# Optimization experiments

Measured on AMD Instinct MI355X. Metric: run time of the kernel, lower is better.

The kernel has to match this reference:

```python
import jax, jax.numpy as jnp
import numpy as np

NUM_HEADS = 16
KEY_DIM = 64
NUM_FEATURES = 256
D_MODEL = NUM_HEADS * KEY_DIM
EPS = 1e-6


def softmax_kernel(data, proj):
    # data: [..., N, D], proj: [D, F]
    # Faithful to source: ratio uses proj.shape[0] (=D), matching the TF code.
    data_normalizer = 1.0 / jnp.sqrt(jnp.sqrt(jnp.asarray(data.shape[-1], data.dtype)))
    ratio = 1.0 / jnp.sqrt(jnp.asarray(proj.shape[0], data.dtype))
    data = data_normalizer * data
    data_dash = jnp.einsum('...nd,df->...nf', data, proj)
    diag = jnp.sum(jnp.square(data), axis=-1, keepdims=True)  # [..., N, 1]
    return ratio * (jnp.exp(data_dash - diag / 2.0) + EPS)


def setup_inputs() -> dict:
    key = jax.random.key(0)
    ks = jax.random.split(key, 12)
    B, N = 4, 4096
    s = 1.0 / np.sqrt(D_MODEL)
    inp = {
        'queries': jax.random.normal(ks[0], (B, N, D_MODEL), jnp.float32),
        'keys': jax.random.normal(ks[1], (B, N, D_MODEL), jnp.float32),
        'Wq': jax.random.normal(ks[2], (D_MODEL, D_MODEL), jnp.float32) * s,
        'bq': jnp.zeros((D_MODEL,), jnp.float32),
        'Wk': jax.random.normal(ks[3], (D_MODEL, D_MODEL), jnp.float32) * s,
        'bk': jnp.zeros((D_MODEL,), jnp.float32),
        'Wv': jax.random.normal(ks[4], (D_MODEL, D_MODEL), jnp.float32) * s,
        'bv': jnp.zeros((D_MODEL,), jnp.float32),
        'Wo': jax.random.normal(ks[5], (D_MODEL, D_MODEL), jnp.float32) * s,
        'bo': jnp.zeros((D_MODEL,), jnp.float32),
        # GlorotNormal for [KEY_DIM, NUM_FEATURES]
        'proj': jax.random.normal(ks[6], (KEY_DIM, NUM_FEATURES), jnp.float32)
                * np.sqrt(2.0 / (KEY_DIM + NUM_FEATURES)),
    }
    return inp


def reference(queries, keys, Wq, bq, Wk, bk, Wv, bv, Wo, bo, proj):
    # Original code uses x = queries for q, k, v (self-attention); keys arg unused.
    x = queries
    B, N, _ = x.shape
    H, D = NUM_HEADS, KEY_DIM

    def split_heads(t):
        return t.reshape(B, N, H, D).transpose(0, 2, 1, 3)  # [B,H,N,D]

    q = split_heads(x @ Wq + bq)
    k = split_heads(x @ Wk + bk)
    v = split_heads(x @ Wv + bv)

    q_prime = softmax_kernel(q, proj)  # [B,H,N,F]
    k_prime = softmax_kernel(k, proj)  # [B,H,N,F]

    kv = jnp.einsum('bhnf,bhnd->bhfd', k_prime, v)        # [B,H,F,D]
    qkv = jnp.einsum('bhnf,bhfd->bhnd', q_prime, kv)       # [B,H,N,D]
    k_sum = jnp.sum(k_prime, axis=2)                        # [B,H,F]
    norm = jnp.einsum('bhnf,bhf->bhn', q_prime, k_sum) + EPS
    qkv = qkv / norm[..., None]

    out = qkv.transpose(0, 2, 1, 3).reshape(B, N, H * D)    # [B,N,d_model]
    return out @ Wo + bo
```

## Files before the change

### kernel.cpp

```cpp
#include <hip/hip_runtime.h>

typedef __attribute__((ext_vector_type(8))) short short8;
typedef __attribute__((ext_vector_type(4))) float f32x4;

#define MFMA16 __builtin_amdgcn_mfma_f32_16x16x32_bf16

#define GLOAD16(gp, lp) __builtin_amdgcn_global_load_lds(                      \
    (const __attribute__((address_space(1))) void*)(gp),                       \
    (__attribute__((address_space(3))) void*)(lp), 16, 0, 0)

__device__ __forceinline__ unsigned short f2bf(float f) {
  unsigned int u = __float_as_uint(f);
  unsigned int r = u + 0x7fffu + ((u >> 16) & 1u);
  return (unsigned short)(r >> 16);
}
__device__ __forceinline__ float bf2f(unsigned short h) {
  return __uint_as_float(((unsigned int)h) << 16);
}

__global__ __launch_bounds__(256) void cast_x_kernel(
    const float* __restrict__ in, unsigned short* __restrict__ out, int n4) {
  int i = blockIdx.x * 256 + threadIdx.x;
  if (i >= n4) return;
  float4 v = reinterpret_cast<const float4*>(in)[i];
  ushort4 o;
  o.x = f2bf(v.x); o.y = f2bf(v.y); o.z = f2bf(v.z); o.w = f2bf(v.w);
  reinterpret_cast<ushort4*>(out)[i] = o;
}

__global__ __launch_bounds__(256) void tcast_f32_kernel(
    const float* __restrict__ in, unsigned short* __restrict__ out, int R, int C) {
  __shared__ float t[64][65];
  int c0 = blockIdx.x * 64, r0 = blockIdx.y * 64;
  int tx = threadIdx.x, ty = threadIdx.y;
#pragma unroll
  for (int i = 0; i < 16; ++i)
    t[ty + 4 * i][tx] = in[(size_t)(r0 + ty + 4 * i) * C + c0 + tx];
  __syncthreads();
#pragma unroll
  for (int i = 0; i < 16; ++i)
    out[(size_t)(c0 + ty + 4 * i) * R + r0 + tx] = f2bf(t[tx][ty + 4 * i]);
}

__global__ __launch_bounds__(256) void t_bf16_kernel(
    const unsigned short* __restrict__ in, unsigned short* __restrict__ out, int R, int C) {
  __shared__ unsigned short t[64][66];
  size_t base = (size_t)blockIdx.z * (size_t)R * (size_t)C;
  int c0 = blockIdx.x * 64, r0 = blockIdx.y * 64;
  int tx = threadIdx.x, ty = threadIdx.y;
#pragma unroll
  for (int i = 0; i < 16; ++i)
    t[ty + 4 * i][tx] = in[base + (size_t)(r0 + ty + 4 * i) * C + c0 + tx];
  __syncthreads();
#pragma unroll
  for (int i = 0; i < 16; ++i)
    out[base + (size_t)(c0 + ty + 4 * i) * R + r0 + tx] = t[tx][ty + 4 * i];
}

template <int OUTF>
__global__ __launch_bounds__(512) void gemm256_kernel(
    const unsigned short* __restrict__ A,
    const unsigned short* W0, const unsigned short* W1, const unsigned short* W2,
    const float* b0, const float* b1, const float* b2,
    void* o0, void* o1, void* o2) {
  constexpr int KD = 1024, ND = 1024, NT = KD / 64;
  const unsigned short* W = W0; const float* bias = b0; void* op = o0;
  if (blockIdx.z == 1) { W = W1; bias = b1; op = o1; }
  else if (blockIdx.z == 2) { W = W2; bias = b2; op = o2; }

  __shared__ unsigned short lsA[2][16384];
  __shared__ unsigned short lsB[2][16384];
  int tid = threadIdx.x;
  int w = tid >> 6, lane = tid & 63;
  int lo = lane & 15, hi = lane >> 4;
  int wr = w >> 2, wc = w & 3;
  int m0 = blockIdx.x * 256, n0 = blockIdx.y * 256;

  int srow = tid >> 3;
  int schunk = (tid & 7) ^ (srow & 7);
  const unsigned short* gA0 = A + (size_t)(m0 + srow) * KD + schunk * 8;
  const unsigned short* gB0 = W + (size_t)(n0 + srow) * KD + schunk * 8;

  f32x4 acc[8][4];
#pragma unroll
  for (int m = 0; m < 8; ++m)
#pragma unroll
    for (int fn = 0; fn < 4; ++fn) acc[m][fn] = (f32x4){0.f, 0.f, 0.f, 0.f};

#pragma unroll
  for (int i = 0; i < 4; ++i)
    GLOAD16(gA0 + (size_t)i * 64 * KD, &lsA[0][i * 4096 + w * 512]);
#pragma unroll
  for (int i = 0; i < 4; ++i)
    GLOAD16(gB0 + (size_t)i * 64 * KD, &lsB[0][i * 4096 + w * 512]);

  for (int t = 0; t < NT; ++t) {
    int buf = t & 1;
    if (t < NT - 1) {
      int kb = (t + 1) * 64;
#pragma unroll
      for (int i = 0; i < 4; ++i)
        GLOAD16(gA0 + (size_t)i * 64 * KD + kb, &lsA[buf ^ 1][i * 4096 + w * 512]);
#pragma unroll
      for (int i = 0; i < 4; ++i)
        GLOAD16(gB0 + (size_t)i * 64 * KD + kb, &lsB[buf ^ 1][i * 4096 + w * 512]);
      __builtin_amdgcn_sched_barrier(0);
      asm volatile("s_waitcnt vmcnt(8)" ::: "memory");
    } else {
      __builtin_amdgcn_sched_barrier(0);
      asm volatile("s_waitcnt vmcnt(0)" ::: "memory");
    }
    __builtin_amdgcn_sched_barrier(0);
    __builtin_amdgcn_s_barrier();
    __builtin_amdgcn_sched_barrier(0);

    short8 bfr[4][2];
#pragma unroll
    for (int fn = 0; fn < 4; ++fn)
#pragma unroll
      for (int ks = 0; ks < 2; ++ks) {
        int col = wc * 64 + fn * 16 + lo;
        bfr[fn][ks] = *reinterpret_cast<const short8*>(
            &lsB[buf][col * 64 + ((ks * 4 + hi) ^ (lo & 7)) * 8]);
      }
    __builtin_amdgcn_s_setprio(1);
#pragma unroll
    for (int mp = 0; mp < 4; ++mp) {
      short8 afr[2][2];
#pragma unroll
      for (int mi = 0; mi < 2; ++mi)
#pragma unroll
        for (int ks = 0; ks < 2; ++ks) {
          int row = wr * 128 + mp * 32 + mi * 16 + lo;
          afr[mi][ks] = *reinterpret_cast<const short8*>(
              &lsA[buf][row * 64 + ((ks * 4 + hi) ^ (lo & 7)) * 8]);
        }
#pragma unroll
      for (int mi = 0; mi < 2; ++mi)
#pragma unroll
        for (int fn = 0; fn < 4; ++fn) {
          acc[mp * 2 + mi][fn] = MFMA16(afr[mi][0], bfr[fn][0], acc[mp * 2 + mi][fn], 0, 0, 0);
          acc[mp * 2 + mi][fn] = MFMA16(afr[mi][1], bfr[fn][1], acc[mp * 2 + mi][fn], 0, 0, 0);
        }
    }
    __builtin_amdgcn_s_setprio(0);
    __builtin_amdgcn_sched_barrier(0);
    __builtin_amdgcn_s_barrier();
    __builtin_amdgcn_sched_barrier(0);
  }

#pragma unroll
  for (int fn = 0; fn < 4; ++fn) {
    int col = n0 + wc * 64 + fn * 16 + lo;
    float bv = bias[col];
#pragma unroll
    for (int m = 0; m < 8; ++m)
#pragma unroll
      for (int j = 0; j < 4; ++j) {
        int row = m0 + wr * 128 + m * 16 + hi * 4 + j;
        float v = acc[m][fn][j] + bv;
        if (OUTF)
          reinterpret_cast<float*>(op)[(size_t)row * ND + col] = v;
        else
          reinterpret_cast<unsigned short*>(op)[(size_t)row * ND + col] = f2bf(v);
      }
  }
}

__global__ __launch_bounds__(256) void kv_fused_kernel(
    const unsigned short* __restrict__ K, const unsigned short* __restrict__ PT,
    const unsigned short* __restrict__ VT,
    float* __restrict__ kvp, float* __restrict__ ksp) {
  __shared__ unsigned short kp[256 * 40];
  int s = blockIdx.x, bh = blockIdx.y, b = bh >> 4, h = bh & 15;
  int tid = threadIdx.x, w = tid >> 6, lane = tid & 63;
  int lo = lane & 15, hi = lane >> 4;
  int f0w = w * 64;

  short8 pb[4][2];
#pragma unroll
  for (int fn = 0; fn < 4; ++fn) {
    int f = f0w + fn * 16 + lo;
    pb[fn][0] = *reinterpret_cast<const short8*>(PT + (size_t)f * 64 + hi * 8);
    pb[fn][1] = *reinterpret_cast<const short8*>(PT + (size_t)f * 64 + 32 + hi * 8);
  }
  const unsigned short* vbase[4];
#pragma unroll
  for (int fn = 0; fn < 4; ++fn)
    vbase[fn] = VT + (size_t)(bh * 64 + fn * 16 + lo) * 4096;

  f32x4 acck[4][4];
#pragma unroll
  for (int fm = 0; fm < 4; ++fm)
#pragma unroll
    for (int fn = 0; fn < 4; ++fn) acck[fm][fn] = (f32x4){0.f, 0.f, 0.f, 0.f};
  float ks[4] = {0.f, 0.f, 0.f, 0.f};

  for (int c = 0; c < 16; ++c) {
    int n0 = s * 512 + c * 32;
    const unsigned short* Ab = K + (size_t)(b * 4096 + n0) * 1024 + h * 64;
    short8 af[2][2];
    float dp[2] = {0.f, 0.f};
#pragma unroll
    for (int fm = 0; fm < 2; ++fm)
#pragma unroll
      for (int kt = 0; kt < 2; ++kt) {
        af[fm][kt] = *reinterpret_cast<const short8*>(
            Ab + (size_t)(fm * 16 + lo) * 1024 + kt * 32 + hi * 8);
#pragma unroll
        for (int j = 0; j < 8; ++j) {
          float qv = bf2f((unsigned short)af[fm][kt][j]);
          dp[fm] += qv * qv;
        }
      }
#pragma unroll
    for (int fm = 0; fm < 2; ++fm) {
      dp[fm] += __shfl_xor(dp[fm], 16);
      dp[fm] += __shfl_xor(dp[fm], 32);
    }
    f32x4 accf[2][4];
#pragma unroll
    for (int fm = 0; fm < 2; ++fm)
#pragma unroll
      for (int fn = 0; fn < 4; ++fn) accf[fm][fn] = (f32x4){0.f, 0.f, 0.f, 0.f};
#pragma unroll
    for (int fn = 0; fn < 4; ++fn) {
      accf[0][fn] = MFMA16(af[0][0], pb[fn][0], accf[0][fn], 0, 0, 0);
      accf[0][fn] = MFMA16(af[0][1], pb[fn][1], accf[0][fn], 0, 0, 0);
      accf[1][fn] = MFMA16(af[1][0], pb[fn][0], accf[1][fn], 0, 0, 0);
      accf[1][fn] = MFMA16(af[1][1], pb[fn][1], accf[1][fn], 0, 0, 0);
    }
#pragma unroll
    for (int fm = 0; fm < 2; ++fm)
#pragma unroll
      for (int fn = 0; fn < 4; ++fn)
#pragma unroll
        for (int j = 0; j < 4; ++j) {
          float dg = __shfl(dp[fm], hi * 4 + j);
          float v = 0.125f *
                    (__expf(0.35355339059327373f * accf[fm][fn][j] - 0.0625f * dg) + 1e-6f);
          ks[fn] += v;
          kp[(f0w + fn * 16 + lo) * 40 + fm * 16 + hi * 4 + j] = f2bf(v);
        }
    short8 a2[4], b2[4];
#pragma unroll
    for (int fm = 0; fm < 4; ++fm)
      a2[fm] = *reinterpret_cast<const short8*>(&kp[(f0w + fm * 16 + lo) * 40 + hi * 8]);
#pragma unroll
    for (int fn = 0; fn < 4; ++fn)
      b2[fn] = *reinterpret_cast<const short8*>(vbase[fn] + n0 + hi * 8);
#pragma unroll
    for (int fm = 0; fm < 4; ++fm)
#pragma unroll
      for (int fn = 0; fn < 4; ++fn)
        acck[fm][fn] = MFMA16(a2[fm], b2[fn], acck[fm][fn], 0, 0, 0);
  }
#pragma unroll
  for (int fn = 0; fn < 4; ++fn) {
    float v = ks[fn];
    v += __shfl_xor(v, 16);
    v += __shfl_xor(v, 32);
    if (hi == 0)
      ksp[(size_t)(s * 64 + bh) * 256 + f0w + fn * 16 + lo] = v;
  }
#pragma unroll
  for (int fm = 0; fm < 4; ++fm)
#pragma unroll
    for (int fn = 0; fn < 4; ++fn)
#pragma unroll
      for (int j = 0; j < 4; ++j)
        kvp[((size_t)(s * 64 + bh) * 256 + f0w + fm * 16 + hi * 4 + j) * 64 + fn * 16 + lo] =
            acck[fm][fn][j];
}

__global__ __launch_bounds__(256) void kvred_kernel(
    const float* __restrict__ kvp, const float* __restrict__ ksp,
    unsigned short* __restrict__ kvT, float* __restrict__ ksum) {
  int bh = blockIdx.x, tid = threadIdx.x;
  for (int i = tid; i < 64 * 256; i += 256) {
    int f = i >> 6, d = i & 63;
    float sum = 0.f;
#pragma unroll
    for (int s = 0; s < 8; ++s)
      sum += kvp[((size_t)(s * 64 + bh) * 256 + f) * 64 + d];
    kvT[(size_t)(bh * 64 + d) * 256 + f] = f2bf(sum);
  }
  {
    float t = 0.f;
#pragma unroll
    for (int s = 0; s < 8; ++s) t += ksp[(size_t)(s * 64 + bh) * 256 + tid];
    ksum[bh * 256 + tid] = t;
  }
}

__global__ __launch_bounds__(256) void qkv_fused_kernel(
    const unsigned short* __restrict__ Q, const unsigned short* __restrict__ PT,
    const unsigned short* __restrict__ KVT, const float* __restrict__ KSUM,
    unsigned short* __restrict__ Y) {
  __shared__ unsigned short qp[128 * 256];
  int bh = blockIdx.y, b = bh >> 4, h = bh & 15;
  int t0 = blockIdx.x * 128;
  int tid = threadIdx.x, w = tid >> 6, lane = tid & 63;
  int lo = lane & 15, hi = lane >> 4;
  int r0 = w * 32;
  const unsigned short* Ab = Q + (size_t)(b * 4096 + t0 + r0) * 1024 + h * 64;

  float ksr[16];
#pragma unroll
  for (int fn = 0; fn < 16; ++fn) ksr[fn] = KSUM[bh * 256 + fn * 16 + lo];

  short8 af[2][2];
  float dp[2] = {0.f, 0.f};
#pragma unroll
  for (int fm = 0; fm < 2; ++fm)
#pragma unroll
    for (int kt = 0; kt < 2; ++kt) {
      af[fm][kt] = *reinterpret_cast<const short8*>(
          Ab + (size_t)(fm * 16 + lo) * 1024 + kt * 32 + hi * 8);
#pragma unroll
      for (int j = 0; j < 8; ++j) {
        float qv = bf2f((unsigned short)af[fm][kt][j]);
        dp[fm] += qv * qv;
      }
    }
#pragma unroll
  for (int fm = 0; fm < 2; ++fm) {
    dp[fm] += __shfl_xor(dp[fm], 16);
    dp[fm] += __shfl_xor(dp[fm], 32);
  }

  float np[2][4] = {{0.f, 0.f, 0.f, 0.f}, {0.f, 0.f, 0.f, 0.f}};
#pragma unroll
  for (int hf = 0; hf < 2; ++hf) {
    f32x4 accf[2][8];
#pragma unroll
    for (int fm = 0; fm < 2; ++fm)
#pragma unroll
      for (int fn = 0; fn < 8; ++fn) accf[fm][fn] = (f32x4){0.f, 0.f, 0.f, 0.f};
#pragma unroll
    for (int fn = 0; fn < 8; ++fn) {
      int f = (hf * 8 + fn) * 16 + lo;
      short8 pb0 = *reinterpret_cast<const short8*>(PT + (size_t)f * 64 + hi * 8);
      short8 pb1 = *reinterpret_cast<const short8*>(PT + (size_t)f * 64 + 32 + hi * 8);
      accf[0][fn] = MFMA16(af[0][0], pb0, accf[0][fn], 0, 0, 0);
      accf[0][fn] = MFMA16(af[0][1], pb1, accf[0][fn], 0, 0, 0);
      accf[1][fn] = MFMA16(af[1][0], pb0, accf[1][fn], 0, 0, 0);
      accf[1][fn] = MFMA16(af[1][1], pb1, accf[1][fn], 0, 0, 0);
    }
#pragma unroll
    for (int fm = 0; fm < 2; ++fm)
#pragma unroll
      for (int fn = 0; fn < 8; ++fn)
#pragma unroll
        for (int j = 0; j < 4; ++j) {
          float dg = __shfl(dp[fm], hi * 4 + j);
          float v = 0.125f *
                    (__expf(0.35355339059327373f * accf[fm][fn][j] - 0.0625f * dg) + 1e-6f);
          np[fm][j] += v * ksr[hf * 8 + fn];
          int row = r0 + fm * 16 + hi * 4 + j;
          int f = (hf * 8 + fn) * 16 + lo;
          int byt = (row * 512 + f * 2) ^ ((row & 7) << 4);
          *reinterpret_cast<unsigned short*>(reinterpret_cast<char*>(qp) + byt) = f2bf(v);
        }
  }
#pragma unroll
  for (int fm = 0; fm < 2; ++fm)
#pragma unroll
    for (int j = 0; j < 4; ++j) {
      np[fm][j] += __shfl_xor(np[fm][j], 1);
      np[fm][j] += __shfl_xor(np[fm][j], 2);
      np[fm][j] += __shfl_xor(np[fm][j], 4);
      np[fm][j] += __shfl_xor(np[fm][j], 8);
    }
  f32x4 acco[2][4];
#pragma unroll
  for (int fm = 0; fm < 2; ++fm)
#pragma unroll
    for (int fn = 0; fn < 4; ++fn) acco[fm][fn] = (f32x4){0.f, 0.f, 0.f, 0.f};
#pragma unroll
  for (int kt2 = 0; kt2 < 8; ++kt2) {
    short8 a2[2], b2[4];
#pragma unroll
    for (int fm = 0; fm < 2; ++fm) {
      int row = r0 + fm * 16 + lo;
      int byt = (row * 512 + kt2 * 64 + hi * 16) ^ ((row & 7) << 4);
      a2[fm] = *reinterpret_cast<const short8*>(reinterpret_cast<char*>(qp) + byt);
    }
#pragma unroll
    for (int fn = 0; fn < 4; ++fn)
      b2[fn] = *reinterpret_cast<const short8*>(
          KVT + (size_t)(bh * 64 + fn * 16 + lo) * 256 + kt2 * 32 + hi * 8);
#pragma unroll
    for (int fm = 0; fm < 2; ++fm)
#pragma unroll
      for (int fn = 0; fn < 4; ++fn)
        acco[fm][fn] = MFMA16(a2[fm], b2[fn], acco[fm][fn], 0, 0, 0);
  }
#pragma unroll
  for (int fm = 0; fm < 2; ++fm)
#pragma unroll
    for (int j = 0; j < 4; ++j) {
      float nv = np[fm][j] + 1e-6f;
      int row = b * 4096 + t0 + r0 + fm * 16 + hi * 4 + j;
#pragma unroll
      for (int fn = 0; fn < 4; ++fn)
        Y[(size_t)row * 1024 + h * 64 + fn * 16 + lo] = f2bf(acco[fm][fn][j] / nv);
    }
}

extern "C" void kernel_launch(void* const* d_in, const int* in_sizes, int n_in,
                              void* d_out, int out_size, void* d_ws, size_t ws_size,
                              hipStream_t stream) {
  (void)in_sizes; (void)n_in; (void)out_size; (void)ws_size;
  const float* x    = (const float*)d_in[0];
  const float* Wq   = (const float*)d_in[2];
  const float* bq   = (const float*)d_in[3];
  const float* Wk   = (const float*)d_in[4];
  const float* bk   = (const float*)d_in[5];
  const float* Wv   = (const float*)d_in[6];
  const float* bv   = (const float*)d_in[7];
  const float* Wo   = (const float*)d_in[8];
  const float* bo   = (const float*)d_in[9];
  const float* proj = (const float*)d_in[10];
  float* out = (float*)d_out;

  constexpr size_t SZ_XB = (size_t)16384 * 1024 * 2;
  constexpr size_t SZ_W  = (size_t)1024 * 1024 * 2;
  constexpr size_t SZ_PT = (size_t)256 * 64 * 2;

  char* p = (char*)d_ws;
  size_t off = 0;
  char* a_xb  = p + off; off += SZ_XB;
  char* a_WqT = p + off; off += SZ_W;
  char* a_WkT = p + off; off += SZ_W;
  char* a_WvT = p + off; off += SZ_W;
  char* a_WoT = p + off; off += SZ_W;
  char* a_pT  = p + off; off += SZ_PT;
  char* a_qb  = p + off; off += SZ_XB;
  char* a_kb  = p + off; off += SZ_XB;
  char* a_ksp  = p + off; off += (size_t)8 * 64 * 256 * 4;
  char* a_kvT  = p + off; off += (size_t)64 * 64 * 256 * 2;
  char* a_ksum = p + off; off += (size_t)64 * 256 * 4;

  char* a_kvp = a_xb;
  char* a_y = a_kb;
  char* a_vb = (char*)d_out;
  char* a_vT = (char*)d_out + SZ_XB;

  dim3 tb(64, 4);

  cast_x_kernel<<<16384, 256, 0, stream>>>(x, (unsigned short*)a_xb, 16384 * 1024 / 4);
  tcast_f32_kernel<<<dim3(16, 16), tb, 0, stream>>>(Wq, (unsigned short*)a_WqT, 1024, 1024);
  tcast_f32_kernel<<<dim3(16, 16), tb, 0, stream>>>(Wk, (unsigned short*)a_WkT, 1024, 1024);
  tcast_f32_kernel<<<dim3(16, 16), tb, 0, stream>>>(Wv, (unsigned short*)a_WvT, 1024, 1024);
  tcast_f32_kernel<<<dim3(16, 16), tb, 0, stream>>>(Wo, (unsigned short*)a_WoT, 1024, 1024);
  tcast_f32_kernel<<<dim3(4, 1), tb, 0, stream>>>(proj, (unsigned short*)a_pT, 64, 256);

  gemm256_kernel<0><<<dim3(64, 4, 3), 512, 0, stream>>>(
      (unsigned short*)a_xb,
      (unsigned short*)a_WqT, (unsigned short*)a_WkT, (unsigned short*)a_WvT,
      bq, bk, bv, a_qb, a_kb, a_vb);

  t_bf16_kernel<<<dim3(16, 64, 4), tb, 0, stream>>>(
      (unsigned short*)a_vb, (unsigned short*)a_vT, 4096, 1024);

  kv_fused_kernel<<<dim3(8, 64), 256, 0, stream>>>(
      (unsigned short*)a_kb, (unsigned short*)a_pT, (unsigned short*)a_vT,
      (float*)a_kvp, (float*)a_ksp);
  kvred_kernel<<<64, 256, 0, stream>>>(
      (float*)a_kvp, (float*)a_ksp, (unsigned short*)a_kvT, (float*)a_ksum);

  qkv_fused_kernel<<<dim3(32, 64), 256, 0, stream>>>(
      (unsigned short*)a_qb, (unsigned short*)a_pT, (unsigned short*)a_kvT,
      (float*)a_ksum, (unsigned short*)a_y);

  gemm256_kernel<1><<<dim3(64, 4, 1), 512, 0, stream>>>(
      (unsigned short*)a_y,
      (unsigned short*)a_WoT, nullptr, nullptr,
      bo, nullptr, nullptr, out, nullptr, nullptr);
}
```

Measured before the change: 353.4 us.

## Deepen GEMM global-to-LDS pipeline to four stages with BK=32 tiles

Changes the 256x256 projection GEMM from double-buffered K=64 tiles to a four-slot ring of K=32 tiles, prefetching three tiles ahead. The LDS swizzle is changed to fit 32-element rows. The aim is to hide global load latency with more loads in flight. In exchange there are twice as many barrier pairs per K loop and half the MFMA work between barriers.

```diff
diff --git a/kernel.cpp b/kernel.cpp
--- a/kernel.cpp
+++ b/kernel.cpp
@@ -63,49 +63,57 @@
     const unsigned short* W0, const unsigned short* W1, const unsigned short* W2,
     const float* b0, const float* b1, const float* b2,
     void* o0, void* o1, void* o2) {
-  constexpr int KD = 1024, ND = 1024, NT = KD / 64;
+  constexpr int KD = 1024, ND = 1024, NT = KD / 32;
   const unsigned short* W = W0; const float* bias = b0; void* op = o0;
   if (blockIdx.z == 1) { W = W1; bias = b1; op = o1; }
   else if (blockIdx.z == 2) { W = W2; bias = b2; op = o2; }
 
-  __shared__ unsigned short lsA[2][16384];
-  __shared__ unsigned short lsB[2][16384];
+  __shared__ unsigned short lsA[4][8192];
+  __shared__ unsigned short lsB[4][8192];
   int tid = threadIdx.x;
   int w = tid >> 6, lane = tid & 63;
   int lo = lane & 15, hi = lane >> 4;
   int wr = w >> 2, wc = w & 3;
   int m0 = blockIdx.x * 256, n0 = blockIdx.y * 256;
 
-  int srow = tid >> 3;
-  int schunk = (tid & 7) ^ (srow & 7);
+  int srow = tid >> 2;
+  int sx = ((tid >> 2) & 3) ^ ((tid >> 4) & 3);
+  int schunk = (tid & 3) ^ sx;
   const unsigned short* gA0 = A + (size_t)(m0 + srow) * KD + schunk * 8;
   const unsigned short* gB0 = W + (size_t)(n0 + srow) * KD + schunk * 8;
 
+#define STAGE_TILE(tt, buf)                                                    \
+  do {                                                                         \
+    int kb_ = (tt) * 32;                                                       \
+    GLOAD16(gA0 + kb_, &lsA[buf][w * 512]);                                    \
+    GLOAD16(gA0 + (size_t)128 * KD + kb_, &lsA[buf][4096 + w * 512]);          \
+    GLOAD16(gB0 + kb_, &lsB[buf][w * 512]);                                    \
+    GLOAD16(gB0 + (size_t)128 * KD + kb_, &lsB[buf][4096 + w * 512]);          \
+  } while (0)
+
   f32x4 acc[8][4];
 #pragma unroll
   for (int m = 0; m < 8; ++m)
 #pragma unroll
     for (int fn = 0; fn < 4; ++fn) acc[m][fn] = (f32x4){0.f, 0.f, 0.f, 0.f};
 
-#pragma unroll
-  for (int i = 0; i < 4; ++i)
-    GLOAD16(gA0 + (size_t)i * 64 * KD, &lsA[0][i * 4096 + w * 512]);
-#pragma unroll
-  for (int i = 0; i < 4; ++i)
-    GLOAD16(gB0 + (size_t)i * 64 * KD, &lsB[0][i * 4096 + w * 512]);
+  STAGE_TILE(0, 0);
+  STAGE_TILE(1, 1);
+  STAGE_TILE(2, 2);
 
   for (int t = 0; t < NT; ++t) {
-    int buf = t & 1;
-    if (t < NT - 1) {
-      int kb = (t + 1) * 64;
-#pragma unroll
-      for (int i = 0; i < 4; ++i)
-        GLOAD16(gA0 + (size_t)i * 64 * KD + kb, &lsA[buf ^ 1][i * 4096 + w * 512]);
-#pragma unroll
-      for (int i = 0; i < 4; ++i)
-        GLOAD16(gB0 + (size_t)i * 64 * KD + kb, &lsB[buf ^ 1][i * 4096 + w * 512]);
+    int buf = t & 3;
+    int rem = NT - 1 - t;
+    if (rem >= 3) {
+      STAGE_TILE(t + 3, (t + 3) & 3);
+      __builtin_amdgcn_sched_barrier(0);
+      asm volatile("s_waitcnt vmcnt(12)" ::: "memory");
+    } else if (rem == 2) {
       __builtin_amdgcn_sched_barrier(0);
       asm volatile("s_waitcnt vmcnt(8)" ::: "memory");
+    } else if (rem == 1) {
+      __builtin_amdgcn_sched_barrier(0);
+      asm volatile("s_waitcnt vmcnt(4)" ::: "memory");
     } else {
       __builtin_amdgcn_sched_barrier(0);
       asm volatile("s_waitcnt vmcnt(0)" ::: "memory");
@@ -114,40 +122,35 @@
     __builtin_amdgcn_s_barrier();
     __builtin_amdgcn_sched_barrier(0);
 
-    short8 bfr[4][2];
-#pragma unroll
-    for (int fn = 0; fn < 4; ++fn)
-#pragma unroll
-      for (int ks = 0; ks < 2; ++ks) {
-        int col = wc * 64 + fn * 16 + lo;
-        bfr[fn][ks] = *reinterpret_cast<const short8*>(
-            &lsB[buf][col * 64 + ((ks * 4 + hi) ^ (lo & 7)) * 8]);
+    short8 bfr[4];
+#pragma unroll
+    for (int fn = 0; fn < 4; ++fn) {
+      int col = wc * 64 + fn * 16 + lo;
+      int cx = (col & 3) ^ ((col >> 2) & 3);
+      bfr[fn] = *reinterpret_cast<const short8*>(&lsB[buf][col * 32 + (hi ^ cx) * 8]);
+    }
+    __builtin_amdgcn_s_setprio(1);
+#pragma unroll
+    for (int mp = 0; mp < 4; ++mp) {
+      short8 afr[2];
+#pragma unroll
+      for (int mi = 0; mi < 2; ++mi) {
+        int row = wr * 128 + mp * 32 + mi * 16 + lo;
+        int rx = (row & 3) ^ ((row >> 2) & 3);
+        afr[mi] = *reinterpret_cast<const short8*>(&lsA[buf][row * 32 + (hi ^ rx) * 8]);
       }
-    __builtin_amdgcn_s_setprio(1);
-#pragma unroll
-    for (int mp = 0; mp < 4; ++mp) {
-      short8 afr[2][2];
 #pragma unroll
       for (int mi = 0; mi < 2; ++mi)
 #pragma unroll
-        for (int ks = 0; ks < 2; ++ks) {
-          int row = wr * 128 + mp * 32 + mi * 16 + lo;
-          afr[mi][ks] = *reinterpret_cast<const short8*>(
-              &lsA[buf][row * 64 + ((ks * 4 + hi) ^ (lo & 7)) * 8]);
-        }
-#pragma unroll
-      for (int mi = 0; mi < 2; ++mi)
-#pragma unroll
-        for (int fn = 0; fn < 4; ++fn) {
-          acc[mp * 2 + mi][fn] = MFMA16(afr[mi][0], bfr[fn][0], acc[mp * 2 + mi][fn], 0, 0, 0);
-          acc[mp * 2 + mi][fn] = MFMA16(afr[mi][1], bfr[fn][1], acc[mp * 2 + mi][fn], 0, 0, 0);
-        }
+        for (int fn = 0; fn < 4; ++fn)
+          acc[mp * 2 + mi][fn] = MFMA16(afr[mi], bfr[fn], acc[mp * 2 + mi][fn], 0, 0, 0);
     }
     __builtin_amdgcn_s_setprio(0);
     __builtin_amdgcn_sched_barrier(0);
     __builtin_amdgcn_s_barrier();
     __builtin_amdgcn_sched_barrier(0);
   }
+#undef STAGE_TILE
 
 #pragma unroll
   for (int fn = 0; fn < 4; ++fn) {
```

Result: slower. 383.6 us (+8.6%).

## Split GEMM K-tiles into half-stages and interleave loads with four MFMA phases

Applied to the files above, without the earlier changes.

Restructures the 256x256 bf16 GEMM main loop so each 64-wide K tile is split into two 32-wide halves, each stored as a separate LDS buffer with a new XOR swizzle. Each iteration runs four compute phases, and the global-to-LDS load for one next-tile quarter is issued before each phase, with finer vmcnt waits. The aim is to overlap global loads with MFMA work more evenly and to cut register pressure by holding fewer A/B fragments at once. In exchange it adds more barriers per iteration and relies on hand-tuned waitcnt counts being correct.

```diff
diff --git a/kernel.cpp b/kernel.cpp
--- a/kernel.cpp
+++ b/kernel.cpp
@@ -68,18 +68,25 @@
   if (blockIdx.z == 1) { W = W1; bias = b1; op = o1; }
   else if (blockIdx.z == 2) { W = W2; bias = b2; op = o2; }
 
-  __shared__ unsigned short lsA[2][16384];
-  __shared__ unsigned short lsB[2][16384];
+  __shared__ unsigned short lsA[2][2][8192];
+  __shared__ unsigned short lsB[2][2][8192];
   int tid = threadIdx.x;
   int w = tid >> 6, lane = tid & 63;
   int lo = lane & 15, hi = lane >> 4;
   int wr = w >> 2, wc = w & 3;
   int m0 = blockIdx.x * 256, n0 = blockIdx.y * 256;
-
-  int srow = tid >> 3;
-  int schunk = (tid & 7) ^ (srow & 7);
-  const unsigned short* gA0 = A + (size_t)(m0 + srow) * KD + schunk * 8;
-  const unsigned short* gB0 = W + (size_t)(n0 + srow) * KD + schunk * 8;
+  int rx = (lo >> 1) & 3;
+
+  int srow = w * 16 + (lane >> 2);
+  int sch = (lane & 3) ^ ((lane >> 3) & 3);
+  const unsigned short* gA = A + (size_t)(m0 + srow) * KD + sch * 8;
+  const unsigned short* gB = W + (size_t)(n0 + srow) * KD + sch * 8;
+
+#define STAGE_HALF(dst, gp, koff)                                              \
+  do {                                                                         \
+    GLOAD16((gp) + (koff), &(dst)[w * 512]);                                   \
+    GLOAD16((gp) + (size_t)128 * KD + (koff), &(dst)[w * 512 + 4096]);         \
+  } while (0)
 
   f32x4 acc[8][4];
 #pragma unroll
@@ -87,67 +94,108 @@
 #pragma unroll
     for (int fn = 0; fn < 4; ++fn) acc[m][fn] = (f32x4){0.f, 0.f, 0.f, 0.f};
 
-#pragma unroll
-  for (int i = 0; i < 4; ++i)
-    GLOAD16(gA0 + (size_t)i * 64 * KD, &lsA[0][i * 4096 + w * 512]);
-#pragma unroll
-  for (int i = 0; i < 4; ++i)
-    GLOAD16(gB0 + (size_t)i * 64 * KD, &lsB[0][i * 4096 + w * 512]);
+  STAGE_HALF(lsA[0][0], gA, 0);
+  STAGE_HALF(lsB[0][0], gB, 0);
+  STAGE_HALF(lsA[0][1], gA, 32);
+  STAGE_HALF(lsB[0][1], gB, 32);
 
   for (int t = 0; t < NT; ++t) {
-    int buf = t & 1;
-    if (t < NT - 1) {
-      int kb = (t + 1) * 64;
-#pragma unroll
-      for (int i = 0; i < 4; ++i)
-        GLOAD16(gA0 + (size_t)i * 64 * KD + kb, &lsA[buf ^ 1][i * 4096 + w * 512]);
-#pragma unroll
-      for (int i = 0; i < 4; ++i)
-        GLOAD16(gB0 + (size_t)i * 64 * KD + kb, &lsB[buf ^ 1][i * 4096 + w * 512]);
-      __builtin_amdgcn_sched_barrier(0);
-      asm volatile("s_waitcnt vmcnt(8)" ::: "memory");
-    } else {
-      __builtin_amdgcn_sched_barrier(0);
-      asm volatile("s_waitcnt vmcnt(0)" ::: "memory");
-    }
-    __builtin_amdgcn_sched_barrier(0);
-    __builtin_amdgcn_s_barrier();
-    __builtin_amdgcn_sched_barrier(0);
-
-    short8 bfr[4][2];
+    int p = t & 1, q = p ^ 1;
+    int kn = (t + 1) * 64;
+    bool more = (t < NT - 1);
+    short8 bf[4], afr[4];
+
+    if (more) STAGE_HALF(lsA[q][0], gA, kn);
+    __builtin_amdgcn_sched_barrier(0);
+    if (more) asm volatile("s_waitcnt vmcnt(6)" ::: "memory");
+    else      asm volatile("s_waitcnt vmcnt(4)" ::: "memory");
+    __builtin_amdgcn_sched_barrier(0);
+    __builtin_amdgcn_s_barrier();
 #pragma unroll
     for (int fn = 0; fn < 4; ++fn)
-#pragma unroll
-      for (int ks = 0; ks < 2; ++ks) {
-        int col = wc * 64 + fn * 16 + lo;
-        bfr[fn][ks] = *reinterpret_cast<const short8*>(
-            &lsB[buf][col * 64 + ((ks * 4 + hi) ^ (lo & 7)) * 8]);
-      }
+      bf[fn] = *reinterpret_cast<const short8*>(
+          &lsB[p][0][(wc * 64 + fn * 16 + lo) * 32 + (hi ^ rx) * 8]);
+#pragma unroll
+    for (int i = 0; i < 4; ++i)
+      afr[i] = *reinterpret_cast<const short8*>(
+          &lsA[p][0][(wr * 128 + i * 16 + lo) * 32 + (hi ^ rx) * 8]);
+    asm volatile("s_waitcnt lgkmcnt(0)" ::: "memory");
+    __builtin_amdgcn_sched_barrier(0);
     __builtin_amdgcn_s_setprio(1);
 #pragma unroll
-    for (int mp = 0; mp < 4; ++mp) {
-      short8 afr[2][2];
-#pragma unroll
-      for (int mi = 0; mi < 2; ++mi)
-#pragma unroll
-        for (int ks = 0; ks < 2; ++ks) {
-          int row = wr * 128 + mp * 32 + mi * 16 + lo;
-          afr[mi][ks] = *reinterpret_cast<const short8*>(
-              &lsA[buf][row * 64 + ((ks * 4 + hi) ^ (lo & 7)) * 8]);
-        }
-#pragma unroll
-      for (int mi = 0; mi < 2; ++mi)
-#pragma unroll
-        for (int fn = 0; fn < 4; ++fn) {
-          acc[mp * 2 + mi][fn] = MFMA16(afr[mi][0], bfr[fn][0], acc[mp * 2 + mi][fn], 0, 0, 0);
-          acc[mp * 2 + mi][fn] = MFMA16(afr[mi][1], bfr[fn][1], acc[mp * 2 + mi][fn], 0, 0, 0);
-        }
-    }
+    for (int i = 0; i < 4; ++i)
+#pragma unroll
+      for (int fn = 0; fn < 4; ++fn)
+        acc[i][fn] = MFMA16(afr[i], bf[fn], acc[i][fn], 0, 0, 0);
     __builtin_amdgcn_s_setprio(0);
     __builtin_amdgcn_sched_barrier(0);
     __builtin_amdgcn_s_barrier();
-    __builtin_amdgcn_sched_barrier(0);
-  }
+
+    if (more) STAGE_HALF(lsB[q][0], gB, kn);
+    __builtin_amdgcn_sched_barrier(0);
+    __builtin_amdgcn_s_barrier();
+#pragma unroll
+    for (int i = 0; i < 4; ++i)
+      afr[i] = *reinterpret_cast<const short8*>(
+          &lsA[p][0][(wr * 128 + 64 + i * 16 + lo) * 32 + (hi ^ rx) * 8]);
+    asm volatile("s_waitcnt lgkmcnt(0)" ::: "memory");
+    __builtin_amdgcn_sched_barrier(0);
+    __builtin_amdgcn_s_setprio(1);
+#pragma unroll
+    for (int i = 0; i < 4; ++i)
+#pragma unroll
+      for (int fn = 0; fn < 4; ++fn)
+        acc[4 + i][fn] = MFMA16(afr[i], bf[fn], acc[4 + i][fn], 0, 0, 0);
+    __builtin_amdgcn_s_setprio(0);
+    __builtin_amdgcn_sched_barrier(0);
+    __builtin_amdgcn_s_barrier();
+
+    if (more) STAGE_HALF(lsA[q][1], gA, kn + 32);
+    __builtin_amdgcn_sched_barrier(0);
+    if (more) asm volatile("s_waitcnt vmcnt(6)" ::: "memory");
+    else      asm volatile("s_waitcnt vmcnt(0)" ::: "memory");
+    __builtin_amdgcn_sched_barrier(0);
+    __builtin_amdgcn_s_barrier();
+#pragma unroll
+    for (int fn = 0; fn < 4; ++fn)
+      bf[fn] = *reinterpret_cast<const short8*>(
+          &lsB[p][1][(wc * 64 + fn * 16 + lo) * 32 + (hi ^ rx) * 8]);
+#pragma unroll
+    for (int i = 0; i < 4; ++i)
+      afr[i] = *reinterpret_cast<const short8*>(
+          &lsA[p][1][(wr * 128 + i * 16 + lo) * 32 + (hi ^ rx) * 8]);
+    asm volatile("s_waitcnt lgkmcnt(0)" ::: "memory");
+    __builtin_amdgcn_sched_barrier(0);
+    __builtin_amdgcn_s_setprio(1);
+#pragma unroll
+    for (int i = 0; i < 4; ++i)
+#pragma unroll
+      for (int fn = 0; fn < 4; ++fn)
+        acc[i][fn] = MFMA16(afr[i], bf[fn], acc[i][fn], 0, 0, 0);
+    __builtin_amdgcn_s_setprio(0);
+    __builtin_amdgcn_sched_barrier(0);
+    __builtin_amdgcn_s_barrier();
+
+    if (more) STAGE_HALF(lsB[q][1], gB, kn + 32);
+    __builtin_amdgcn_sched_barrier(0);
+    __builtin_amdgcn_s_barrier();
+#pragma unroll
+    for (int i = 0; i < 4; ++i)
+      afr[i] = *reinterpret_cast<const short8*>(
+          &lsA[p][1][(wr * 128 + 64 + i * 16 + lo) * 32 + (hi ^ rx) * 8]);
+    asm volatile("s_waitcnt lgkmcnt(0)" ::: "memory");
+    __builtin_amdgcn_sched_barrier(0);
+    __builtin_amdgcn_s_setprio(1);
+#pragma unroll
+    for (int i = 0; i < 4; ++i)
+#pragma unroll
+      for (int fn = 0; fn < 4; ++fn)
+        acc[4 + i][fn] = MFMA16(afr[i], bf[fn], acc[4 + i][fn], 0, 0, 0);
+    __builtin_amdgcn_s_setprio(0);
+    __builtin_amdgcn_sched_barrier(0);
+    __builtin_amdgcn_s_barrier();
+  }
+#undef STAGE_HALF
 
 #pragma unroll
   for (int fn = 0; fn < 4; ++fn) {
```

Result: slower. 370.4 us (+4.8%).
